# Optimization experiments

Hardware: AMD Instinct MI355X
Metric: run time of the kernel (lower is better)

Reference implementation:

```python
import jax, jax.numpy as jnp
import numpy as np

ALPHA = 1.0
EPS = 1e-09
N_PATCH = 128


def _triplet_loss(xp, xn, alpha, eps):
    # xp, xn: [B, N, D], assumed L2-normalized rows
    n = xp.shape[1]
    p_dist = 2.0 - 2.0 * jnp.einsum('bnd,bmd->bnm', xp, xp)   # [B,N,N]
    pn_dist = 2.0 - 2.0 * jnp.einsum('bnd,bmd->bnm', xp, xn)  # [B,N,N]
    # ppn_dist[b,i,j,k] = alpha + p_dist[b,i,j] - pn_dist[b,i,k]
    ppn = alpha + p_dist[:, :, :, None] - pn_dist[:, :, None, :]  # [B,N,N,N]
    mask = ppn <= 0
    pos = jnp.where(mask, 0.0, ppn)
    num = jnp.sum(pos, axis=-1)                                # [B,N,N]
    den = n - jnp.sum(mask, axis=-1).astype(pos.dtype) + eps   # [B,N,N]
    return jnp.mean(num / den)


def setup_inputs() -> dict:
    key = jax.random.key(0)
    latent = jax.random.normal(key, (8192, 512), dtype=jnp.float32)
    return {"latent": latent}


def reference(latent):
    bsz = latent.shape[0] // (2 * N_PATCH)
    latent = latent / jnp.linalg.norm(latent, axis=-1, keepdims=True)
    latent = latent.reshape(bsz, 2, N_PATCH, -1)
    t_latent, c_latent = latent[:, 0], latent[:, 1]
    loss = _triplet_loss(t_latent, c_latent, ALPHA, EPS) + _triplet_loss(c_latent, t_latent, ALPHA, EPS)
    return loss
```

## Files before the change

### kernel.cpp

```cpp
#include <hip/hip_runtime.h>
#include <hip/hip_bf16.h>

constexpr int   D      = 512;
constexpr float ALPHA  = 1.0f;
constexpr float EPS    = 1e-9f;
constexpr float INV_CNT = 1.0f / (32.0f * 128.0f * 128.0f);

constexpr size_t NRM_OFF  = 0;
constexpr size_t PART_OFF = 8388608;

typedef short bf16x8 __attribute__((ext_vector_type(8)));
typedef float f32x4  __attribute__((ext_vector_type(4)));

__device__ __forceinline__ short f2bf(float f) {
    unsigned u = __builtin_bit_cast(unsigned, f);
    unsigned r = (u + 0x7FFFu + ((u >> 16) & 1u)) >> 16;
    return (short)r;
}


__global__ __launch_bounds__(256) void k_normalize(const float* __restrict__ in,
                                                   short* __restrict__ nrm2) {
    const int wid  = threadIdx.x >> 6;
    const int lane = threadIdx.x & 63;
    const int p    = blockIdx.x;
    const int r    = (p & 7) * 1024 + (p >> 3) * 4 + wid;
    const int b    = r >> 8;
    const int row  = r & 255;
    const float4* src = (const float4*)(in + (size_t)r * D);
    float4 x0 = src[2 * lane];
    float4 x1 = src[2 * lane + 1];
    float ss = x0.x*x0.x + x0.y*x0.y + x0.z*x0.z + x0.w*x0.w
             + x1.x*x1.x + x1.y*x1.y + x1.z*x1.z + x1.w*x1.w;
    #pragma unroll
    for (int o = 32; o > 0; o >>= 1) ss += __shfl_xor(ss, o, 64);
    const float inv = rsqrtf(ss);
    bf16x8 v;
    v[0] = f2bf(x0.x * inv); v[1] = f2bf(x0.y * inv);
    v[2] = f2bf(x0.z * inv); v[3] = f2bf(x0.w * inv);
    v[4] = f2bf(x1.x * inv); v[5] = f2bf(x1.y * inv);
    v[6] = f2bf(x1.z * inv); v[7] = f2bf(x1.w * inv);
    const int ks   = lane >> 2;
    const int slot = ((lane & 3) + (row >> 1)) & 3;
    char* dst = (char*)nrm2 + ((((size_t)b * 16 + ks) * 256 + row) * 64 + slot * 16);
    *(bf16x8*)dst = v;
}

constexpr int PSTR = 260;

__global__ __launch_bounds__(256, 4) void k_fused(const short* __restrict__ nrm2,
                                                  float* __restrict__ part) {
    __shared__ __align__(16) char smem[16672];

    const int p     = blockIdx.x;
    const int slot  = p >> 3;
    const int b     = (p & 7) * 4 + (slot & 3);
    const int rem   = slot >> 2;
    const int chunk = rem & 7;
    const int half  = rem >> 3;
    const int w     = threadIdx.x >> 6;
    const int lane  = threadIdx.x & 63;
    const int fr    = lane & 15;
    const int kg    = lane >> 4;

    const char* batchbase = (const char*)nrm2 + (size_t)b * 16 * 256 * 64;

    const int sigma = (kg + (fr >> 1)) & 3;

    const int Arow = half * 128 + chunk * 16 + fr;
    const char* gA = batchbase + Arow * 64 + sigma * 16;

    const char* gB0 = batchbase + (w * 64 +  0 + fr) * 64 + sigma * 16;
    const char* gB1 = gB0 + 16 * 64;
    const char* gB2 = gB0 + 32 * 64;
    const char* gB3 = gB0 + 48 * 64;

    f32x4 acc0 = {0.f,0.f,0.f,0.f}, acc1 = {0.f,0.f,0.f,0.f};
    f32x4 acc2 = {0.f,0.f,0.f,0.f}, acc3 = {0.f,0.f,0.f,0.f};

    #pragma unroll
    for (int s = 0; s < 16; s++) {
        const size_t o = (size_t)s * 16384;
        const bf16x8 a  = *(const bf16x8*)(gA  + o);
        const bf16x8 b0 = *(const bf16x8*)(gB0 + o);
        const bf16x8 b1 = *(const bf16x8*)(gB1 + o);
        const bf16x8 b2 = *(const bf16x8*)(gB2 + o);
        const bf16x8 b3 = *(const bf16x8*)(gB3 + o);
        acc0 = __builtin_amdgcn_mfma_f32_16x16x32_bf16(a, b0, acc0, 0, 0, 0);
        acc1 = __builtin_amdgcn_mfma_f32_16x16x32_bf16(a, b1, acc1, 0, 0, 0);
        acc2 = __builtin_amdgcn_mfma_f32_16x16x32_bf16(a, b2, acc2, 0, 0, 0);
        acc3 = __builtin_amdgcn_mfma_f32_16x16x32_bf16(a, b3, acc3, 0, 0, 0);
    }

    float* P   = (float*)smem;
    float* red = (float*)&smem[16640];

    {
        const int rw = kg * 4;
        const int cw = w * 64 + fr;
        #pragma unroll
        for (int q = 0; q < 4; q++) P[(rw + q) * PSTR + cw]      = acc0[q];
        #pragma unroll
        for (int q = 0; q < 4; q++) P[(rw + q) * PSTR + cw + 16] = acc1[q];
        #pragma unroll
        for (int q = 0; q < 4; q++) P[(rw + q) * PSTR + cw + 32] = acc2[q];
        #pragma unroll
        for (int q = 0; q < 4; q++) P[(rw + q) * PSTR + cw + 48] = acc3[q];
    }
    __syncthreads();

    const int pd_off = half ? 128 : 0;
    const int pn_off = 128 - pd_off;
    float wacc = 0.f;
    #pragma unroll
    for (int rr = 0; rr < 4; rr++) {
        const int r = w * 4 + rr;
        float* prow = &P[r * PSTR];

        const float g0 = prow[pd_off + lane];
        const float g1 = prow[pd_off + lane + 64];
        float v0 = prow[pn_off + lane];
        float v1 = prow[pn_off + lane + 64];

        #pragma unroll
        for (int kk = 2; kk <= 128; kk <<= 1) {
            if (kk == 128) {
                const float lo = fminf(v0, v1);
                const float hi = fmaxf(v0, v1);
                v0 = lo; v1 = hi;
            }
            #pragma unroll
            for (int j = (kk == 128 ? 32 : (kk >> 1)); j >= 1; j >>= 1) {
                const float p0 = __shfl_xor(v0, j, 64);
                const float p1 = __shfl_xor(v1, j, 64);
                const bool up0 = (lane & kk) == 0;
                const bool up1 = ((lane + 64) & kk) == 0;
                const bool lower = (lane & j) == 0;
                v0 = (up0 == lower) ? fminf(v0, p0) : fmaxf(v0, p0);
                v1 = (up1 == lower) ? fminf(v1, p1) : fmaxf(v1, p1);
            }
        }

        float inc0 = v0, inc1 = v1;
        #pragma unroll
        for (int o = 1; o < 64; o <<= 1) {
            const float t0 = __shfl_up(inc0, o, 64);
            const float t1 = __shfl_up(inc1, o, 64);
            if (lane >= o) { inc0 += t0; inc1 += t1; }
        }
        const float tot0  = __shfl(inc0, 63, 64);
        const float total = tot0 + __shfl(inc1, 63, 64);

        prow[lane]            = v0;
        prow[64 + lane]       = v1;
        prow[130 + 1 + lane]  = inc0;
        prow[130 + 65 + lane] = tot0 + inc1;
        if (lane == 0) prow[130] = 0.f;

        #pragma unroll
        for (int h = 0; h < 2; h++) {
            const float g   = h ? g1 : g0;
            const float tau = g - 0.5f * ALPHA;
            const float a   = ALPHA - 2.f * g;
            int pos = 0;
            #pragma unroll
            for (int st = 128; st > 0; st >>= 1) {
                const int nidx = pos + st;
                const float sv = prow[nidx - 1];
                pos = ((nidx <= 128) && (sv <= tau)) ? nidx : pos;
            }
            const float cnt = (float)(128 - pos);
            const float pre = prow[130 + pos];
            const float num = cnt * a + 2.f * (total - pre);
            wacc += num / (cnt + EPS);
        }
    }

    #pragma unroll
    for (int o = 32; o > 0; o >>= 1) wacc += __shfl_xor(wacc, o, 64);
    if (lane == 0) red[w] = wacc;
    __syncthreads();
    if (threadIdx.x == 0)
        part[p] = red[0] + red[1] + red[2] + red[3];
}

__global__ __launch_bounds__(512) void k_reduce(const float* __restrict__ part,
                                                float* __restrict__ out) {
    __shared__ float red[8];
    const int w    = threadIdx.x >> 6;
    const int lane = threadIdx.x & 63;
    float s = part[threadIdx.x];
    #pragma unroll
    for (int o = 32; o > 0; o >>= 1) s += __shfl_xor(s, o, 64);
    if (lane == 0) red[w] = s;
    __syncthreads();
    if (threadIdx.x == 0) {
        float t = 0.f;
        #pragma unroll
        for (int i = 0; i < 8; i++) t += red[i];
        out[0] = t * INV_CNT;
    }
}

extern "C" void kernel_launch(void* const* d_in, const int* in_sizes, int n_in,
                              void* d_out, int out_size, void* d_ws, size_t ws_size,
                              hipStream_t stream) {
    const float* latent = (const float*)d_in[0];
    float* out  = (float*)d_out;
    char*  wsb  = (char*)d_ws;
    short* nrm2 = (short*)(wsb + NRM_OFF);
    float* part = (float*)(wsb + PART_OFF);

    hipLaunchKernelGGL(k_normalize, dim3(2048), dim3(256), 0, stream, latent, nrm2);
    hipLaunchKernelGGL(k_fused,     dim3(512),  dim3(256), 0, stream, nrm2, part);
    hipLaunchKernelGGL(k_reduce,    dim3(1),    dim3(512), 0, stream, part, out);
}
```

Before: 30.52 us.

## Merge both triplet directions into one 512-thread block sharing B-operand loads

Each fused block now computes both the t-anchor and c-anchor 16-row chunks for a batch. Eight waves each own 32 columns, and every loaded B fragment feeds two MFMAs. The grid halves to 256 blocks of 512 threads, so B-operand global loads are shared across the two halves and the partial count shrinks. In exchange, LDS per block doubles and fewer blocks run, which lowers parallelism on a GPU with many CUs.

```diff
diff --git a/kernel.cpp b/kernel.cpp
--- a/kernel.cpp
+++ b/kernel.cpp
@@ -48,16 +48,14 @@
 
 constexpr int PSTR = 260;
 
-__global__ __launch_bounds__(256, 4) void k_fused(const short* __restrict__ nrm2,
+__global__ __launch_bounds__(512, 2) void k_fused(const short* __restrict__ nrm2,
                                                   float* __restrict__ part) {
-    __shared__ __align__(16) char smem[16672];
+    __shared__ __align__(16) char smem[33312];
 
     const int p     = blockIdx.x;
     const int slot  = p >> 3;
     const int b     = (p & 7) * 4 + (slot & 3);
-    const int rem   = slot >> 2;
-    const int chunk = rem & 7;
-    const int half  = rem >> 3;
+    const int chunk = slot >> 2;
     const int w     = threadIdx.x >> 6;
     const int lane  = threadIdx.x & 63;
     const int fr    = lane & 15;
@@ -67,54 +65,50 @@
 
     const int sigma = (kg + (fr >> 1)) & 3;
 
-    const int Arow = half * 128 + chunk * 16 + fr;
-    const char* gA = batchbase + Arow * 64 + sigma * 16;
-
-    const char* gB0 = batchbase + (w * 64 +  0 + fr) * 64 + sigma * 16;
+    const char* gAt = batchbase + (chunk * 16 + fr) * 64 + sigma * 16;
+    const char* gAc = gAt + 128 * 64;
+    const char* gB0 = batchbase + (w * 32 + fr) * 64 + sigma * 16;
     const char* gB1 = gB0 + 16 * 64;
-    const char* gB2 = gB0 + 32 * 64;
-    const char* gB3 = gB0 + 48 * 64;
-
-    f32x4 acc0 = {0.f,0.f,0.f,0.f}, acc1 = {0.f,0.f,0.f,0.f};
-    f32x4 acc2 = {0.f,0.f,0.f,0.f}, acc3 = {0.f,0.f,0.f,0.f};
+
+    f32x4 accT0 = {0.f,0.f,0.f,0.f}, accT1 = {0.f,0.f,0.f,0.f};
+    f32x4 accC0 = {0.f,0.f,0.f,0.f}, accC1 = {0.f,0.f,0.f,0.f};
 
     #pragma unroll
     for (int s = 0; s < 16; s++) {
         const size_t o = (size_t)s * 16384;
-        const bf16x8 a  = *(const bf16x8*)(gA  + o);
+        const bf16x8 at = *(const bf16x8*)(gAt + o);
+        const bf16x8 ac = *(const bf16x8*)(gAc + o);
         const bf16x8 b0 = *(const bf16x8*)(gB0 + o);
         const bf16x8 b1 = *(const bf16x8*)(gB1 + o);
-        const bf16x8 b2 = *(const bf16x8*)(gB2 + o);
-        const bf16x8 b3 = *(const bf16x8*)(gB3 + o);
-        acc0 = __builtin_amdgcn_mfma_f32_16x16x32_bf16(a, b0, acc0, 0, 0, 0);
-        acc1 = __builtin_amdgcn_mfma_f32_16x16x32_bf16(a, b1, acc1, 0, 0, 0);
-        acc2 = __builtin_amdgcn_mfma_f32_16x16x32_bf16(a, b2, acc2, 0, 0, 0);
-        acc3 = __builtin_amdgcn_mfma_f32_16x16x32_bf16(a, b3, acc3, 0, 0, 0);
+        accT0 = __builtin_amdgcn_mfma_f32_16x16x32_bf16(at, b0, accT0, 0, 0, 0);
+        accT1 = __builtin_amdgcn_mfma_f32_16x16x32_bf16(at, b1, accT1, 0, 0, 0);
+        accC0 = __builtin_amdgcn_mfma_f32_16x16x32_bf16(ac, b0, accC0, 0, 0, 0);
+        accC1 = __builtin_amdgcn_mfma_f32_16x16x32_bf16(ac, b1, accC1, 0, 0, 0);
     }
 
     float* P   = (float*)smem;
-    float* red = (float*)&smem[16640];
+    float* red = (float*)&smem[33280];
 
     {
         const int rw = kg * 4;
-        const int cw = w * 64 + fr;
-        #pragma unroll
-        for (int q = 0; q < 4; q++) P[(rw + q) * PSTR + cw]      = acc0[q];
-        #pragma unroll
-        for (int q = 0; q < 4; q++) P[(rw + q) * PSTR + cw + 16] = acc1[q];
-        #pragma unroll
-        for (int q = 0; q < 4; q++) P[(rw + q) * PSTR + cw + 32] = acc2[q];
-        #pragma unroll
-        for (int q = 0; q < 4; q++) P[(rw + q) * PSTR + cw + 48] = acc3[q];
+        const int cw = w * 32 + fr;
+        #pragma unroll
+        for (int q = 0; q < 4; q++) P[(rw + q) * PSTR + cw]           = accT0[q];
+        #pragma unroll
+        for (int q = 0; q < 4; q++) P[(rw + q) * PSTR + cw + 16]      = accT1[q];
+        #pragma unroll
+        for (int q = 0; q < 4; q++) P[(16 + rw + q) * PSTR + cw]      = accC0[q];
+        #pragma unroll
+        for (int q = 0; q < 4; q++) P[(16 + rw + q) * PSTR + cw + 16] = accC1[q];
     }
     __syncthreads();
 
-    const int pd_off = half ? 128 : 0;
-    const int pn_off = 128 - pd_off;
     float wacc = 0.f;
     #pragma unroll
     for (int rr = 0; rr < 4; rr++) {
-        const int r = w * 4 + rr;
+        const int r      = w * 4 + rr;
+        const int pd_off = (r < 16) ? 0 : 128;
+        const int pn_off = 128 - pd_off;
         float* prow = &P[r * PSTR];
 
         const float g0 = prow[pd_off + lane];
@@ -180,13 +174,17 @@
     for (int o = 32; o > 0; o >>= 1) wacc += __shfl_xor(wacc, o, 64);
     if (lane == 0) red[w] = wacc;
     __syncthreads();
-    if (threadIdx.x == 0)
-        part[p] = red[0] + red[1] + red[2] + red[3];
-}
-
-__global__ __launch_bounds__(512) void k_reduce(const float* __restrict__ part,
+    if (threadIdx.x == 0) {
+        float s = 0.f;
+        #pragma unroll
+        for (int i = 0; i < 8; i++) s += red[i];
+        part[p] = s;
+    }
+}
+
+__global__ __launch_bounds__(256) void k_reduce(const float* __restrict__ part,
                                                 float* __restrict__ out) {
-    __shared__ float red[8];
+    __shared__ float red[4];
     const int w    = threadIdx.x >> 6;
     const int lane = threadIdx.x & 63;
     float s = part[threadIdx.x];
@@ -194,12 +192,8 @@
     for (int o = 32; o > 0; o >>= 1) s += __shfl_xor(s, o, 64);
     if (lane == 0) red[w] = s;
     __syncthreads();
-    if (threadIdx.x == 0) {
-        float t = 0.f;
-        #pragma unroll
-        for (int i = 0; i < 8; i++) t += red[i];
-        out[0] = t * INV_CNT;
-    }
+    if (threadIdx.x == 0)
+        out[0] = (red[0] + red[1] + red[2] + red[3]) * INV_CNT;
 }
 
 extern "C" void kernel_launch(void* const* d_in, const int* in_sizes, int n_in,
@@ -212,6 +206,6 @@
     float* part = (float*)(wsb + PART_OFF);
 
     hipLaunchKernelGGL(k_normalize, dim3(2048), dim3(256), 0, stream, latent, nrm2);
-    hipLaunchKernelGGL(k_fused,     dim3(512),  dim3(256), 0, stream, nrm2, part);
-    hipLaunchKernelGGL(k_reduce,    dim3(1),    dim3(512), 0, stream, part, out);
-}
+    hipLaunchKernelGGL(k_fused,     dim3(256),  dim3(512), 0, stream, nrm2, part);
+    hipLaunchKernelGGL(k_reduce,    dim3(1),    dim3(256), 0, stream, part, out);
+}
```

Measured after the change: 29.23 us, median of 2. -4.2%, faster.
